# Kernel tuning notes

Hardware: AMD Instinct MI355X
Metric: run time of the kernel (lower is better)

The kernel has to match this reference:

```python
import jax, jax.numpy as jnp
import numpy as np

HIDDEN = 512
HEADS = 8
HEAD_DIM = HIDDEN // HEADS   # 64
MAN_DIM = 256                # manifold_dim = hidden_dim // 2
SCALE = HEAD_DIM ** -0.5


def _c(re, im):
    return jax.lax.complex(re, im)


def setup_inputs() -> dict:
    key = jax.random.key(0)
    ks = jax.random.split(key, 13)
    def w(k, shape, fan_in):
        return (jax.random.normal(k, shape, dtype=jnp.float32) / np.sqrt(fan_in)).astype(jnp.float32)
    B, S = 2, 2048
    return {
        "x": jax.random.normal(ks[0], (B, S, HIDDEN), dtype=jnp.float32),
        "Wq_re": w(ks[1], (HIDDEN, HIDDEN), HIDDEN), "Wq_im": w(ks[2], (HIDDEN, HIDDEN), HIDDEN),
        "Wk_re": w(ks[3], (HIDDEN, HIDDEN), HIDDEN), "Wk_im": w(ks[4], (HIDDEN, HIDDEN), HIDDEN),
        "Wv_re": w(ks[5], (HIDDEN, HIDDEN), HIDDEN), "Wv_im": w(ks[6], (HIDDEN, HIDDEN), HIDDEN),
        "Wm_re": w(ks[7], (HEAD_DIM, MAN_DIM), HEAD_DIM), "Wm_im": w(ks[8], (HEAD_DIM, MAN_DIM), HEAD_DIM),
        "Wmi_re": w(ks[9], (MAN_DIM, HEAD_DIM), MAN_DIM), "Wmi_im": w(ks[10], (MAN_DIM, HEAD_DIM), MAN_DIM),
        "Wo_re": w(ks[11], (HIDDEN, HIDDEN), HIDDEN), "Wo_im": w(ks[12], (HIDDEN, HIDDEN), HIDDEN),
    }


def reference(x, Wq_re, Wq_im, Wk_re, Wk_im, Wv_re, Wv_im,
              Wm_re, Wm_im, Wmi_re, Wmi_im, Wo_re, Wo_im):
    B, S, D = x.shape
    # quantum state preparation: cast to complex, L2-normalize along last dim
    xc = x.astype(jnp.complex64)
    norm = jnp.linalg.norm(xc, axis=-1, keepdims=True)
    xc = xc / norm

    Wq, Wk, Wv = _c(Wq_re, Wq_im), _c(Wk_re, Wk_im), _c(Wv_re, Wv_im)
    Wm, Wmi, Wo = _c(Wm_re, Wm_im), _c(Wmi_re, Wmi_im), _c(Wo_re, Wo_im)

    def heads(t):  # [B,S,D] -> [B,H,S,head_dim]
        return t.reshape(B, S, HEADS, HEAD_DIM).transpose(0, 2, 1, 3)

    q = heads(xc @ Wq)
    k = heads(xc @ Wk)
    v = heads(xc @ Wv)

    # project each head onto the manifold (complex linear)
    qm = jnp.einsum('bhsd,dm->bhsm', q, Wm)
    km = jnp.einsum('bhsd,dm->bhsm', k, Wm)
    vm = jnp.einsum('bhsd,dm->bhsm', v, Wm)

    # Hermitian inner product attention scores; softmax over real part
    scores = jnp.einsum('bhqm,bhkm->bhqk', qm, jnp.conj(km)) * SCALE
    attn = jax.nn.softmax(scores.real, axis=-1).astype(jnp.complex64)

    outm = jnp.einsum('bhqk,bhkm->bhqm', attn, vm)
    out = jnp.einsum('bhsm,md->bhsd', outm, Wmi)        # back to head_dim
    out = out.transpose(0, 2, 1, 3).reshape(B, S, D)    # merge heads
    out = out @ Wo
    # return real/imag stacked as float32 (complex64 output -> [B,S,D,2])
    return jnp.stack([out.real, out.imag], axis=-1)
```

## Files before the change

kernel.cpp:

```cpp
#include <hip/hip_runtime.h>
#include <hip/hip_bf16.h>
#include <stdint.h>


typedef __attribute__((ext_vector_type(8))) short bf16x8;
typedef __attribute__((ext_vector_type(4))) float f32x4;

#define QSCALE 0.18033688011112042f

__device__ __forceinline__ unsigned short f2b(float f) {
    union { float f; unsigned int u; } v; v.f = f;
    unsigned int r = v.u + 0x7fffu + ((v.u >> 16) & 1u);
    return (unsigned short)(r >> 16);
}

__device__ __forceinline__ float b2f(short s) {
    union { float f; unsigned int u; } v;
    v.u = ((unsigned int)(unsigned short)s) << 16;
    return v.f;
}

__device__ __forceinline__ unsigned int cvtpk(float a, float b) {
    union { __hip_bfloat162 h; unsigned int u; } v;
    v.h = __float22bfloat162_rn(make_float2(a, b));
    return v.u;
}

__device__ __forceinline__ void ld16(void* lds, const void* g) {
    __builtin_amdgcn_global_load_lds(
        (__attribute__((address_space(1))) unsigned int*)(g),
        (__attribute__((address_space(3))) unsigned int*)(lds), 16, 0, 0);
}

__device__ __forceinline__ void plswap32(unsigned int& a, unsigned int& b) {
#if __has_builtin(__builtin_amdgcn_permlane32_swap)
    auto r = __builtin_amdgcn_permlane32_swap(a, b, false, false);
    a = r[0]; b = r[1];
#else
    asm("s_nop 0\n\tv_permlane32_swap_b32 %0, %1" : "+v"(a), "+v"(b));
#endif
}

__device__ __forceinline__ void plswap16(unsigned int& a, unsigned int& b) {
#if __has_builtin(__builtin_amdgcn_permlane16_swap)
    auto r = __builtin_amdgcn_permlane16_swap(a, b, false, false);
    a = r[0]; b = r[1];
#else
    asm("s_nop 0\n\tv_permlane16_swap_b32 %0, %1" : "+v"(a), "+v"(b));
#endif
}

__global__ __launch_bounds__(256) void k_prep(
        const float* __restrict__ x, unsigned short* __restrict__ xn,
        const float* __restrict__ Wq_re, const float* __restrict__ Wq_im,
        const float* __restrict__ Wk_re, const float* __restrict__ Wk_im,
        const float* __restrict__ Wv_re, const float* __restrict__ Wv_im,
        const float* __restrict__ Wm_re, const float* __restrict__ Wm_im,
        unsigned short* __restrict__ WqkvT, unsigned short* __restrict__ Bq,
        float* __restrict__ WmT_re, float* __restrict__ WmT_im) {
    __shared__ float tile[64][65];
    if (blockIdx.x < 1024) {
        int row  = blockIdx.x * 4 + (threadIdx.x >> 6);
        int lane = threadIdx.x & 63;
        const float4* xr = (const float4*)(x + (size_t)row * 512);
        float4 a = xr[lane], b = xr[lane + 64];
        float s = a.x*a.x + a.y*a.y + a.z*a.z + a.w*a.w
                + b.x*b.x + b.y*b.y + b.z*b.z + b.w*b.w;
        #pragma unroll
        for (int m = 1; m < 64; m <<= 1) s += __shfl_xor(s, m, 64);
        float inv = 1.0f / sqrtf(s);
        ushort4 o;
        o.x = f2b(a.x*inv); o.y = f2b(a.y*inv); o.z = f2b(a.z*inv); o.w = f2b(a.w*inv);
        *(ushort4*)&xn[(size_t)row*512 + lane*4] = o;
        o.x = f2b(b.x*inv); o.y = f2b(b.y*inv); o.z = f2b(b.z*inv); o.w = f2b(b.w*inv);
        *(ushort4*)&xn[(size_t)row*512 + 256 + lane*4] = o;
        return;
    }
    int bid = blockIdx.x - 1024;
    int tx = threadIdx.x & 63, ty = threadIdx.x >> 6;
    if (bid < 256) {
        int mat = bid >> 6, tl = bid & 63;
        const float* src = (mat==0)?Wk_re:(mat==1)?Wk_im:(mat==2)?Wv_re:Wv_im;
        int r0 = (tl >> 3) * 64, c0 = (tl & 7) * 64;
        #pragma unroll
        for (int i = 0; i < 16; i++) {
            int r = ty + i*4;
            tile[r][tx] = src[(size_t)(r0 + r)*512 + c0 + tx];
        }
        __syncthreads();
        int sec = 1024 + (mat >> 1)*1024, part = mat & 1;
        #pragma unroll
        for (int i = 0; i < 16; i++) {
            int r = ty + i*4;
            int rr = c0 + r, h = rr >> 6, j = rr & 63;
            WqkvT[(size_t)(sec + h*128 + part*64 + j)*512 + r0 + tx] = f2b(tile[tx][r]);
        }
    } else if (bid < 264) {
        int mat = (bid - 256) >> 2, tl = (bid - 256) & 3;
        const float* src = mat ? Wm_im : Wm_re;
        float* dst = mat ? WmT_im : WmT_re;
        int c0 = tl * 64;
        #pragma unroll
        for (int i = 0; i < 16; i++) {
            int r = ty + i*4;
            tile[r][tx] = src[(size_t)r*256 + c0 + tx];
        }
        __syncthreads();
        #pragma unroll
        for (int i = 0; i < 16; i++) {
            int r = ty + i*4;
            dst[(size_t)(c0 + r)*64 + tx] = tile[tx][r];
        }
    } else {
        int b3 = bid - 264;
        int mat = b3 >> 6, tl = b3 & 63;
        const float* src = mat ? Wq_im : Wq_re;
        #pragma unroll
        for (int i = 0; i < 16; i++) {
            int idx = tl*4096 + i*256 + threadIdx.x;
            int k = idx >> 9, col = idx & 511;
            int h = col >> 6, d = col & 63;
            Bq[(size_t)(h*512 + k)*128 + mat*64 + d] = f2b(src[(size_t)k*512 + col]);
        }
    }
}

__global__ __launch_bounds__(256) void k_gh(const float* __restrict__ Wm_re, const float* __restrict__ Wm_im,
                                            const float* __restrict__ WmT_re, const float* __restrict__ WmT_im,
                                            const float* __restrict__ Wmi_re, const float* __restrict__ Wmi_im,
                                            float* __restrict__ GH, unsigned short* __restrict__ Aq) {
    int id = blockIdx.x * 256 + threadIdx.x;
    int mat = id >> 12;
    int a = (id >> 6) & 63, c = id & 63;
    float s = 0.f;
    if (mat < 2) {
        for (int m = 0; m < 256; m++) {
            float ar = Wm_re[a*256+m], ai = Wm_im[a*256+m];
            float br = WmT_re[m*64+c], bi = WmT_im[m*64+c];
            s += (mat == 0) ? (ar*br + ai*bi) : (ai*br - ar*bi);
        }
        float sq = s * QSCALE;
        if (mat == 0) {
            Aq[c*128 + a]           = f2b(sq);
            Aq[(64+c)*128 + 64 + a] = f2b(sq);
        } else {
            Aq[(64+c)*128 + a]      = f2b(sq);
            Aq[c*128 + 64 + a]      = f2b(-sq);
        }
    } else {
        for (int m = 0; m < 256; m++) {
            float ar = Wm_re[a*256+m], ai = Wm_im[a*256+m];
            float br = Wmi_re[m*64+c], bi = Wmi_im[m*64+c];
            s += (mat == 2) ? (ar*br - ai*bi) : (ar*bi + ai*br);
        }
        GH[mat*4096 + c*64 + a] = s;
    }
}

__global__ __launch_bounds__(256) void k_packwo(
        const float* __restrict__ Wo_re,  const float* __restrict__ Wo_im,
        const float* __restrict__ GH, unsigned short* __restrict__ Wbig) {
    int id = blockIdx.x * 256 + threadIdx.x;
    int np = id >> 10, kk = id & 1023;
    int c = np >> 1, p = np & 1;
    int h = kk >> 7, pp = (kk >> 6) & 1, d = kk & 63;
    const float* HrT = GH + 2*4096;
    const float* HiT = GH + 3*4096;
    float s = 0.f;
    if (p == pp) {
        for (int j = 0; j < 64; j++) {
            float hr = HrT[j*64+d], hi = HiT[j*64+d];
            float wr = Wo_re[(size_t)(h*64+j)*512 + c];
            float wi = Wo_im[(size_t)(h*64+j)*512 + c];
            s += hr*wr - hi*wi;
        }
    } else {
        for (int j = 0; j < 64; j++) {
            float hr = HrT[j*64+d], hi = HiT[j*64+d];
            float wr = Wo_re[(size_t)(h*64+j)*512 + c];
            float wi = Wo_im[(size_t)(h*64+j)*512 + c];
            s += hr*wi + hi*wr;
        }
        if (p == 0) s = -s;
    }
    Wbig[(size_t)np*1024 + kk] = f2b(s);
}

template<int MODE, int MT, int MW>
__global__ __launch_bounds__(256, MW) void k_gemm(
        const unsigned short* __restrict__ Ain, const unsigned short* __restrict__ Btin,
        void* __restrict__ Cout, unsigned short* __restrict__ Vt, int K) {
    __shared__ __align__(16) unsigned short Al[2][MT*32];
    __shared__ __align__(16) unsigned short Bl[2][128*32];
    const int t = threadIdx.x;
    const int wave = t >> 6, lane = t & 63, quad = lane >> 4, l16 = lane & 15;
    const int wr = wave >> 1, wc = wave & 1;

    const unsigned short* A;
    const unsigned short* Bt;
    unsigned short* Cb = nullptr;
    int m0, n0;
    if (MODE == 0) {
        if (blockIdx.y < 16) {
            A = Ain; Bt = Btin;
            m0 = blockIdx.x * 128; n0 = blockIdx.y * 128;
            Cb = (unsigned short*)Cout;
        } else {
            int idx = (blockIdx.y - 16) * 32 + blockIdx.x;
            int b = idx >> 7, mt = (idx >> 4) & 7, nt = idx & 15;
            A  = Btin + 2048*512;
            Bt = Ain + (size_t)b*2048*512;
            m0 = mt * 128; n0 = nt * 128;
            Cb = Vt + (size_t)b*1024*2048;
        }
    } else {
        A = Ain; Bt = Btin;
        m0 = blockIdx.x * MT; n0 = blockIdx.y * 128;
    }

    f32x4 acc[MT/32][4] = {};
    for (int kt = 0; kt < K; kt += 64) {
        #pragma unroll
        for (int kh = 0; kh < 2; kh++)
            #pragma unroll
            for (int i = 0; i < MT/64; i++) {
                int g = t + i*256, r = g >> 2, gr = g & 3;
                ld16(&Al[kh][g*8], &A[(size_t)(m0 + r)*K + kt + kh*32 + gr*8]);
            }
        #pragma unroll
        for (int kh = 0; kh < 2; kh++)
            #pragma unroll
            for (int i = 0; i < 2; i++) {
                int g = t + i*256, r = g >> 2, gr = g & 3;
                ld16(&Bl[kh][g*8], &Bt[(size_t)(n0 + r)*K + kt + kh*32 + gr*8]);
            }
        __syncthreads();
        #pragma unroll
        for (int kh = 0; kh < 2; kh++) {
            bf16x8 af[MT/32], bfr[4];
            #pragma unroll
            for (int rt = 0; rt < MT/32; rt++)
                af[rt] = *(const bf16x8*)&Al[kh][(wr*(MT/2) + rt*16 + l16)*32 + quad*8];
            #pragma unroll
            for (int ct = 0; ct < 4; ct++)
                bfr[ct] = *(const bf16x8*)&Bl[kh][(wc*64 + ct*16 + l16)*32 + quad*8];
            #pragma unroll
            for (int rt = 0; rt < MT/32; rt++)
                #pragma unroll
                for (int ct = 0; ct < 4; ct++)
                    acc[rt][ct] = __builtin_amdgcn_mfma_f32_16x16x32_bf16(af[rt], bfr[ct], acc[rt][ct], 0, 0, 0);
        }
        __syncthreads();
    }
    #pragma unroll
    for (int rt = 0; rt < MT/32; rt++) {
        int row = m0 + wr*(MT/2) + rt*16 + quad*4;
        #pragma unroll
        for (int ct = 0; ct < 4; ct++) {
            int col = n0 + wc*64 + ct*16 + l16;
            if (MODE == 0) {
                unsigned int u01 = cvtpk(acc[rt][ct][0], acc[rt][ct][1]);
                unsigned int u23 = cvtpk(acc[rt][ct][2], acc[rt][ct][3]);
                Cb[(size_t)(row+0)*2048 + col] = (unsigned short)(u01);
                Cb[(size_t)(row+1)*2048 + col] = (unsigned short)(u01 >> 16);
                Cb[(size_t)(row+2)*2048 + col] = (unsigned short)(u23);
                Cb[(size_t)(row+3)*2048 + col] = (unsigned short)(u23 >> 16);
            } else if (MODE == 2) {
                unsigned short* Cq = (unsigned short*)Cout;
                int h = col >> 9, k = col & 511;
                unsigned int u01 = cvtpk(acc[rt][ct][0], acc[rt][ct][1]);
                unsigned int u23 = cvtpk(acc[rt][ct][2], acc[rt][ct][3]);
                Cq[(size_t)(h*128 + row + 0)*512 + k] = (unsigned short)(u01);
                Cq[(size_t)(h*128 + row + 1)*512 + k] = (unsigned short)(u01 >> 16);
                Cq[(size_t)(h*128 + row + 2)*512 + k] = (unsigned short)(u23);
                Cq[(size_t)(h*128 + row + 3)*512 + k] = (unsigned short)(u23 >> 16);
            } else {
                float* C = (float*)Cout;
                #pragma unroll
                for (int r = 0; r < 4; r++)
                    C[(size_t)(row + r)*1024 + col] = acc[rt][ct][r];
            }
        }
    }
}

__global__ __launch_bounds__(256, 3) void k_attn(
        const unsigned short* __restrict__ QK,
        const unsigned short* __restrict__ Vt,
        unsigned short* __restrict__ Opart,
        float* __restrict__ Lpart) {
    __shared__ __align__(16) unsigned short Kl[2][4096];
    __shared__ __align__(16) unsigned short Vl[2][4096];

    const int t = threadIdx.x, w = t >> 6, lane = t & 63, quad = lane >> 4, l16 = lane & 15;
    const int qxr = quad ^ ((l16 >> 2) & 3);
    const int bh = blockIdx.x, b = bh >> 3, h = bh & 7;
    const int qb = blockIdx.y & 15, q4 = blockIdx.y >> 4;
    const int tok0 = b*2048 + qb*128;

    bf16x8 qf[2][4];
    #pragma unroll
    for (int rt = 0; rt < 2; rt++)
        #pragma unroll
        for (int ks = 0; ks < 4; ks++)
            qf[rt][ks] = *(const bf16x8*)&QK[(size_t)(tok0 + w*32 + rt*16 + l16)*2048 + h*128 + ks*32 + quad*8];

    const int kr = (t >> 2) & 31;
    const int kqo = (t & 3) ^ ((kr >> 2) & 3);
    const unsigned short* kp = QK + (size_t)(b*2048 + q4*512 + kr)*2048 + 1024 + h*128 + (t >> 7)*32 + kqo*8;
    const int vd = t >> 2;
    const int vqo = (t & 3) ^ ((vd >> 2) & 3);
    const unsigned short* vp = Vt + (size_t)(b*1024 + h*128 + vd)*2048 + q4*512 + vqo*8;

    f32x4 Oacc[2][8] = {};
    float ls[2] = {};

    ld16(&Kl[0][t*8], kp);
    ld16(&Kl[0][(t+256)*8], kp + 64);
    ld16(&Vl[0][t*8], vp);
    ld16(&Vl[0][(t+256)*8], vp + 131072);
    __syncthreads();

    for (int it = 0; it < 16; it++) {
        const int cur = it & 1;
        if (it < 15) {
            const unsigned short* kp2 = kp + (size_t)(it + 1)*65536;
            const unsigned short* vp2 = vp + (it + 1)*32;
            ld16(&Kl[cur^1][t*8], kp2);
            ld16(&Kl[cur^1][(t+256)*8], kp2 + 64);
            ld16(&Vl[cur^1][t*8], vp2);
            ld16(&Vl[cur^1][(t+256)*8], vp2 + 131072);
        }

        f32x4 S[2][2] = {};
        #pragma unroll
        for (int ks = 0; ks < 4; ks++) {
            bf16x8 kf0 = *(const bf16x8*)&Kl[cur][ks*1024 + l16*32 + qxr*8];
            bf16x8 kf1 = *(const bf16x8*)&Kl[cur][ks*1024 + (16 + l16)*32 + qxr*8];
            #pragma unroll
            for (int rt = 0; rt < 2; rt++) {
                S[rt][0] = __builtin_amdgcn_mfma_f32_16x16x32_bf16(kf0, qf[rt][ks], S[rt][0], 0, 0, 0);
                S[rt][1] = __builtin_amdgcn_mfma_f32_16x16x32_bf16(kf1, qf[rt][ks], S[rt][1], 0, 0, 0);
            }
        }

        bf16x8 pf[2];
        #pragma unroll
        for (int rt = 0; rt < 2; rt++) {
            float p0 = exp2f(S[rt][0][0]), p1 = exp2f(S[rt][0][1]);
            float p2 = exp2f(S[rt][0][2]), p3 = exp2f(S[rt][0][3]);
            float p4 = exp2f(S[rt][1][0]), p5 = exp2f(S[rt][1][1]);
            float p6 = exp2f(S[rt][1][2]), p7 = exp2f(S[rt][1][3]);
            ls[rt] += ((p0 + p1) + (p2 + p3)) + ((p4 + p5) + (p6 + p7));
            unsigned int a0 = cvtpk(p0, p1), c0 = cvtpk(p2, p3);
            unsigned int a1 = cvtpk(p4, p5), c1 = cvtpk(p6, p7);
            plswap32(a0, a1); plswap16(a0, a1);
            plswap32(c0, c1); plswap16(c0, c1);
            union { unsigned int u[4]; bf16x8 v; } pk;
            pk.u[0] = a0; pk.u[1] = c0; pk.u[2] = a1; pk.u[3] = c1;
            pf[rt] = pk.v;
        }

        #pragma unroll
        for (int dt = 0; dt < 8; dt++) {
            bf16x8 vf = *(const bf16x8*)&Vl[cur][(dt*16 + l16)*32 + qxr*8];
            #pragma unroll
            for (int rt = 0; rt < 2; rt++)
                Oacc[rt][dt] = __builtin_amdgcn_mfma_f32_16x16x32_bf16(pf[rt], vf, Oacc[rt][dt], 0, 0, 0);
        }
        __syncthreads();
    }

    unsigned short* Op = Opart + (size_t)q4*4194304;
    float* Lp = Lpart + (size_t)q4*32768;
    #pragma unroll
    for (int rt = 0; rt < 2; rt++) {
        float lt = ls[rt];
        lt += __shfl_xor(lt, 16, 64);
        lt += __shfl_xor(lt, 32, 64);
        if (lane < 16)
            Lp[(size_t)(tok0 + w*32 + rt*16 + l16)*8 + h] = lt;
        float inv[4];
        #pragma unroll
        for (int r = 0; r < 4; r++)
            inv[r] = 1.0f / __shfl(lt, quad*4 + r, 64);
        #pragma unroll
        for (int dt = 0; dt < 8; dt++) {
            int col = h*128 + dt*16 + l16;
            #pragma unroll
            for (int r = 0; r < 4; r++)
                Op[(size_t)(tok0 + w*32 + rt*16 + quad*4 + r)*1024 + col] = f2b(Oacc[rt][dt][r] * inv[r]);
        }
    }
}

__global__ __launch_bounds__(256) void k_merge(const unsigned short* __restrict__ Opart,
                                               const float* __restrict__ Lpart,
                                               unsigned short* __restrict__ O) {
    int slot = blockIdx.x * 256 + threadIdx.x;
    int tok = slot >> 7, colg = slot & 127, h = colg >> 4;
    float l0 = Lpart[(size_t)tok*8 + h];
    float l1 = Lpart[32768  + (size_t)tok*8 + h];
    float l2 = Lpart[65536  + (size_t)tok*8 + h];
    float l3 = Lpart[98304  + (size_t)tok*8 + h];
    float inv = 1.0f / (l0 + l1 + l2 + l3);
    float w0 = l0*inv, w1 = l1*inv, w2 = l2*inv, w3 = l3*inv;
    size_t off = (size_t)tok*1024 + colg*8;
    bf16x8 a0 = *(const bf16x8*)&Opart[off];
    bf16x8 a1 = *(const bf16x8*)&Opart[4194304  + off];
    bf16x8 a2 = *(const bf16x8*)&Opart[8388608  + off];
    bf16x8 a3 = *(const bf16x8*)&Opart[12582912 + off];
    float o[8];
    #pragma unroll
    for (int j = 0; j < 8; j++)
        o[j] = w0*b2f(a0[j]) + w1*b2f(a1[j]) + w2*b2f(a2[j]) + w3*b2f(a3[j]);
    uint4 uo;
    uo.x = cvtpk(o[0], o[1]); uo.y = cvtpk(o[2], o[3]);
    uo.z = cvtpk(o[4], o[5]); uo.w = cvtpk(o[6], o[7]);
    *(uint4*)&O[off] = uo;
}

extern "C" void kernel_launch(void* const* d_in, const int* in_sizes, int n_in,
                              void* d_out, int out_size, void* d_ws, size_t ws_size,
                              hipStream_t stream) {
    (void)in_sizes; (void)n_in; (void)out_size; (void)ws_size;
    const float* x      = (const float*)d_in[0];
    const float* Wq_re  = (const float*)d_in[1];
    const float* Wq_im  = (const float*)d_in[2];
    const float* Wk_re  = (const float*)d_in[3];
    const float* Wk_im  = (const float*)d_in[4];
    const float* Wv_re  = (const float*)d_in[5];
    const float* Wv_im  = (const float*)d_in[6];
    const float* Wm_re  = (const float*)d_in[7];
    const float* Wm_im  = (const float*)d_in[8];
    const float* Wmi_re = (const float*)d_in[9];
    const float* Wmi_im = (const float*)d_in[10];
    const float* Wo_re  = (const float*)d_in[11];
    const float* Wo_im  = (const float*)d_in[12];

    char* ws = (char*)d_ws;
    unsigned short* xn    = (unsigned short*)(ws);
    unsigned short* WqkvT = (unsigned short*)(ws + (4u << 20));
    unsigned short* Wbig  = (unsigned short*)(ws + (7u << 20));
    float*          GH    = (float*)         (ws + (9u << 20));
    float*          WmT_re= (float*)         (ws + (9u << 20) + (64u << 10));
    float*          WmT_im= (float*)         (ws + (9u << 20) + (128u << 10));
    unsigned short* Aq    = (unsigned short*)(ws + (9u << 20) + (192u << 10));
    unsigned short* QK    = (unsigned short*)(ws + (10u << 20));
    unsigned short* Bq    = (unsigned short*)(ws + (10u << 20));
    unsigned short* Vt    = (unsigned short*)(ws + (26u << 20));
    unsigned short* Obuf  = (unsigned short*)(ws + (34u << 20));
    unsigned short* Opart = (unsigned short*)(ws + (42u << 20));
    float*          Lpart = (float*)         (ws + (74u << 20));

    k_prep         <<<dim3(1416), dim3(256), 0, stream>>>(
        x, xn, Wq_re, Wq_im, Wk_re, Wk_im, Wv_re, Wv_im, Wm_re, Wm_im,
        WqkvT, Bq, WmT_re, WmT_im);
    k_gh           <<<dim3(64),   dim3(256), 0, stream>>>(
        Wm_re, Wm_im, WmT_re, WmT_im, Wmi_re, Wmi_im, GH, Aq);
    k_gemm<2,128,2><<<dim3(1, 32),  dim3(256), 0, stream>>>(Aq, Bq, (void*)WqkvT, nullptr, 128);
    k_packwo       <<<dim3(4096), dim3(256), 0, stream>>>(Wo_re, Wo_im, GH, Wbig);
    k_gemm<0,128,3><<<dim3(32, 24), dim3(256), 0, stream>>>(xn, WqkvT, (void*)QK, Vt, 512);
    k_attn         <<<dim3(16, 64), dim3(256), 0, stream>>>(QK, Vt, Opart, Lpart);
    k_merge        <<<dim3(2048), dim3(256), 0, stream>>>(Opart, Lpart, Obuf);
    k_gemm<1,64,2> <<<dim3(64, 8),  dim3(256), 0, stream>>>(Obuf, Wbig, d_out, nullptr, 1024);
}
```

Measured before the change: 239.3 us.

## Fold Gram-matrix kernel into prep kernel and raise wave priority around MFMAs

```diff
diff --git a/kernel.cpp b/kernel.cpp
--- a/kernel.cpp
+++ b/kernel.cpp
@@ -56,8 +56,9 @@
         const float* __restrict__ Wk_re, const float* __restrict__ Wk_im,
         const float* __restrict__ Wv_re, const float* __restrict__ Wv_im,
         const float* __restrict__ Wm_re, const float* __restrict__ Wm_im,
+        const float* __restrict__ Wmi_re, const float* __restrict__ Wmi_im,
         unsigned short* __restrict__ WqkvT, unsigned short* __restrict__ Bq,
-        float* __restrict__ WmT_re, float* __restrict__ WmT_im) {
+        float* __restrict__ GH, unsigned short* __restrict__ Aq) {
     __shared__ float tile[64][65];
     if (blockIdx.x < 1024) {
         int row  = blockIdx.x * 4 + (threadIdx.x >> 6);
@@ -95,24 +96,8 @@
             int rr = c0 + r, h = rr >> 6, j = rr & 63;
             WqkvT[(size_t)(sec + h*128 + part*64 + j)*512 + r0 + tx] = f2b(tile[tx][r]);
         }
-    } else if (bid < 264) {
-        int mat = (bid - 256) >> 2, tl = (bid - 256) & 3;
-        const float* src = mat ? Wm_im : Wm_re;
-        float* dst = mat ? WmT_im : WmT_re;
-        int c0 = tl * 64;
-        #pragma unroll
-        for (int i = 0; i < 16; i++) {
-            int r = ty + i*4;
-            tile[r][tx] = src[(size_t)r*256 + c0 + tx];
-        }
-        __syncthreads();
-        #pragma unroll
-        for (int i = 0; i < 16; i++) {
-            int r = ty + i*4;
-            dst[(size_t)(c0 + r)*64 + tx] = tile[tx][r];
-        }
-    } else {
-        int b3 = bid - 264;
+    } else if (bid < 384) {
+        int b3 = bid - 256;
         int mat = b3 >> 6, tl = b3 & 63;
         const float* src = mat ? Wq_im : Wq_re;
         #pragma unroll
@@ -122,38 +107,33 @@
             int h = col >> 6, d = col & 63;
             Bq[(size_t)(h*512 + k)*128 + mat*64 + d] = f2b(src[(size_t)k*512 + col]);
         }
-    }
-}
-
-__global__ __launch_bounds__(256) void k_gh(const float* __restrict__ Wm_re, const float* __restrict__ Wm_im,
-                                            const float* __restrict__ WmT_re, const float* __restrict__ WmT_im,
-                                            const float* __restrict__ Wmi_re, const float* __restrict__ Wmi_im,
-                                            float* __restrict__ GH, unsigned short* __restrict__ Aq) {
-    int id = blockIdx.x * 256 + threadIdx.x;
-    int mat = id >> 12;
-    int a = (id >> 6) & 63, c = id & 63;
-    float s = 0.f;
-    if (mat < 2) {
-        for (int m = 0; m < 256; m++) {
-            float ar = Wm_re[a*256+m], ai = Wm_im[a*256+m];
-            float br = WmT_re[m*64+c], bi = WmT_im[m*64+c];
-            s += (mat == 0) ? (ar*br + ai*bi) : (ai*br - ar*bi);
-        }
-        float sq = s * QSCALE;
-        if (mat == 0) {
-            Aq[c*128 + a]           = f2b(sq);
-            Aq[(64+c)*128 + 64 + a] = f2b(sq);
+    } else {
+        int id = (bid - 384) * 256 + threadIdx.x;
+        int mat = id >> 12;
+        int a = (id >> 6) & 63, c = id & 63;
+        float s = 0.f;
+        if (mat < 2) {
+            for (int m = 0; m < 256; m++) {
+                float ar = Wm_re[a*256+m], ai = Wm_im[a*256+m];
+                float br = Wm_re[c*256+m], bi = Wm_im[c*256+m];
+                s += (mat == 0) ? (ar*br + ai*bi) : (ai*br - ar*bi);
+            }
+            float sq = s * QSCALE;
+            if (mat == 0) {
+                Aq[c*128 + a]           = f2b(sq);
+                Aq[(64+c)*128 + 64 + a] = f2b(sq);
+            } else {
+                Aq[(64+c)*128 + a]      = f2b(sq);
+                Aq[c*128 + 64 + a]      = f2b(-sq);
+            }
         } else {
-            Aq[(64+c)*128 + a]      = f2b(sq);
-            Aq[c*128 + 64 + a]      = f2b(-sq);
-        }
-    } else {
-        for (int m = 0; m < 256; m++) {
-            float ar = Wm_re[a*256+m], ai = Wm_im[a*256+m];
-            float br = Wmi_re[m*64+c], bi = Wmi_im[m*64+c];
-            s += (mat == 2) ? (ar*br - ai*bi) : (ar*bi + ai*br);
-        }
-        GH[mat*4096 + c*64 + a] = s;
+            for (int m = 0; m < 256; m++) {
+                float ar = Wm_re[a*256+m], ai = Wm_im[a*256+m];
+                float br = Wmi_re[m*64+c], bi = Wmi_im[m*64+c];
+                s += (mat == 2) ? (ar*br - ai*bi) : (ar*bi + ai*br);
+            }
+            GH[mat*4096 + c*64 + a] = s;
+        }
     }
 }
 
@@ -333,6 +313,7 @@
         }
 
         f32x4 S[2][2] = {};
+        __builtin_amdgcn_s_setprio(1);
         #pragma unroll
         for (int ks = 0; ks < 4; ks++) {
             bf16x8 kf0 = *(const bf16x8*)&Kl[cur][ks*1024 + l16*32 + qxr*8];
@@ -343,6 +324,7 @@
                 S[rt][1] = __builtin_amdgcn_mfma_f32_16x16x32_bf16(kf1, qf[rt][ks], S[rt][1], 0, 0, 0);
             }
         }
+        __builtin_amdgcn_s_setprio(0);
 
         bf16x8 pf[2];
         #pragma unroll
@@ -361,6 +343,7 @@
             pf[rt] = pk.v;
         }
 
+        __builtin_amdgcn_s_setprio(1);
         #pragma unroll
         for (int dt = 0; dt < 8; dt++) {
             bf16x8 vf = *(const bf16x8*)&Vl[cur][(dt*16 + l16)*32 + qxr*8];
@@ -368,6 +351,7 @@
             for (int rt = 0; rt < 2; rt++)
                 Oacc[rt][dt] = __builtin_amdgcn_mfma_f32_16x16x32_bf16(pf[rt], vf, Oacc[rt][dt], 0, 0, 0);
         }
+        __builtin_amdgcn_s_setprio(0);
         __syncthreads();
     }
 
@@ -443,8 +427,6 @@
     unsigned short* WqkvT = (unsigned short*)(ws + (4u << 20));
     unsigned short* Wbig  = (unsigned short*)(ws + (7u << 20));
     float*          GH    = (float*)         (ws + (9u << 20));
-    float*          WmT_re= (float*)         (ws + (9u << 20) + (64u << 10));
-    float*          WmT_im= (float*)         (ws + (9u << 20) + (128u << 10));
     unsigned short* Aq    = (unsigned short*)(ws + (9u << 20) + (192u << 10));
     unsigned short* QK    = (unsigned short*)(ws + (10u << 20));
     unsigned short* Bq    = (unsigned short*)(ws + (10u << 20));
@@ -453,11 +435,9 @@
     unsigned short* Opart = (unsigned short*)(ws + (42u << 20));
     float*          Lpart = (float*)         (ws + (74u << 20));
 
-    k_prep         <<<dim3(1416), dim3(256), 0, stream>>>(
+    k_prep         <<<dim3(1472), dim3(256), 0, stream>>>(
         x, xn, Wq_re, Wq_im, Wk_re, Wk_im, Wv_re, Wv_im, Wm_re, Wm_im,
-        WqkvT, Bq, WmT_re, WmT_im);
-    k_gh           <<<dim3(64),   dim3(256), 0, stream>>>(
-        Wm_re, Wm_im, WmT_re, WmT_im, Wmi_re, Wmi_im, GH, Aq);
+        Wmi_re, Wmi_im, WqkvT, Bq, GH, Aq);
     k_gemm<2,128,2><<<dim3(1, 32),  dim3(256), 0, stream>>>(Aq, Bq, (void*)WqkvT, nullptr, 128);
     k_packwo       <<<dim3(4096), dim3(256), 0, stream>>>(Wo_re, Wo_im, GH, Wbig);
     k_gemm<0,128,3><<<dim3(32, 24), dim3(256), 0, stream>>>(xn, WqkvT, (void*)QK, Vt, 512);
```

Result: no change. 234.8 us (-1.9%).
